# Performance work log

Measured on AMD Instinct MI355X. Metric: run time of the kernel, lower is better.

## Reference

```python
import jax, jax.numpy as jnp
import numpy as np
from jax.scipy.linalg import solve_triangular

H, VD, M = 16, 64, 128
RIDGE = 0.01


def setup_inputs() -> dict:
    key = jax.random.key(0)
    ks = jax.random.split(key, 9)
    B, L, HD = 4, 2048, 1024
    s = 1.0 / np.sqrt(HD).astype(np.float32)
    return {
        "x": jax.random.normal(ks[0], (B, L, HD), dtype=jnp.float32),
        "cur_k": jnp.zeros((1,), dtype=jnp.float32),
        "input_mask": jnp.ones((B, L), dtype=jnp.float32),
        "Wq": jax.random.normal(ks[1], (HD, HD), dtype=jnp.float32) * s,
        "Wk": jax.random.normal(ks[2], (HD, HD), dtype=jnp.float32) * s,
        "Wv": jax.random.normal(ks[3], (HD, HD), dtype=jnp.float32) * s,
        "Wo": jax.random.normal(ks[4], (HD, HD), dtype=jnp.float32) * s,
        "bo": jax.random.normal(ks[5], (HD,), dtype=jnp.float32) * s,
        "rff_W": jax.random.normal(ks[6], (H, VD, M), dtype=jnp.float32),  # / lengthscale=1.0
        "rff_b": 2.0 * np.pi * jax.random.uniform(ks[7], (H, M), dtype=jnp.float32),
    }


def reference(x, cur_k, input_mask, Wq, Wk, Wv, Wo, bo, rff_W, rff_b):
    B, L, HD = x.shape
    scale = jnp.asarray(1.0 / np.sqrt(M), dtype=x.dtype)
    M2 = 2 * M

    def heads(t):  # [B,L,HD] -> [B,H,L,VD]
        return t.reshape(B, L, H, VD).transpose(0, 2, 1, 3)

    q = heads(x @ Wq.T)
    k = heads(x @ Wk.T)
    v = heads(x @ Wv.T)

    mask = input_mask[:, :L].astype(x.dtype)
    qmask = mask[:, None, :, None]  # [B,1,L,1]

    def rff(X):  # [B,H,L,VD] -> [B,H,L,2M]
        proj = jnp.einsum('bhld,hdm->bhlm', X, rff_W) + rff_b[None, :, None, :]
        return scale * jnp.concatenate([jnp.cos(proj), jnp.sin(proj)], axis=-1)

    PhiQ = rff(q)
    PhiK_w = rff(k) * qmask
    V_w = v * qmask

    G = jnp.einsum('bhlm,bhln->bhmn', PhiK_w, PhiK_w)  # [B,H,2M,2M]
    G = G + RIDGE * jnp.eye(M2, dtype=x.dtype)
    T = jnp.einsum('bhlm,bhld->bhmd', PhiK_w, V_w)      # [B,H,2M,VD]

    Lch = jnp.linalg.cholesky(G)
    y = solve_triangular(Lch, T, lower=True)
    W = solve_triangular(jnp.swapaxes(Lch, -2, -1), y, lower=False)

    out = jnp.einsum('bhlm,bhmd->bhld', PhiQ, W)        # [B,H,L,VD]
    # unsqueeze sample dim, permute to [B,1,L,H,VD], flatten heads -> [B,1,L,HD]
    samples = jnp.transpose(out, (0, 2, 1, 3)).reshape(B, L, HD)[:, None]
    samples = samples @ Wo.T + bo                        # W_O (dropout: eval no-op)
    samples = samples * qmask                            # [B,1,L,1] broadcast
    return samples
```

## Files before the change

### kernel.cpp

```cpp
#include <hip/hip_runtime.h>
#include <math.h>

#define B_ 4
#define L_ 2048
#define HD_ 1024
#define H_ 16
#define VD_ 64
#define M_ 128
#define M2_ 256
#define RIDGE_ 0.01f
#define SCALE_ 0.08838834764831845f

typedef unsigned short u16;
typedef __attribute__((ext_vector_type(8))) short short8;
typedef __attribute__((ext_vector_type(4))) float floatx4;

__device__ __forceinline__ u16 f2bf(float x) {
  unsigned u = __float_as_uint(x);
  unsigned r = u + 0x7fff + ((u >> 16) & 1);
  return (u16)(r >> 16);
}
__device__ __forceinline__ float bf2f(u16 h) {
  return __uint_as_float(((unsigned)h) << 16);
}
__device__ __forceinline__ void gload_lds16(const u16* g, u16* l) {
  __builtin_amdgcn_global_load_lds(
      (const __attribute__((address_space(1))) unsigned int*)g,
      (__attribute__((address_space(3))) unsigned int*)l, 16, 0, 0);
}
__device__ __forceinline__ void split4(float4 f, ushort4* h, float4* r) {
  h->x = f2bf(f.x); h->y = f2bf(f.y); h->z = f2bf(f.z); h->w = f2bf(f.w);
  r->x = f.x - bf2f(h->x); r->y = f.y - bf2f(h->y);
  r->z = f.z - bf2f(h->z); r->w = f.w - bf2f(h->w);
}

__global__ __launch_bounds__(256) void cvt_split_kernel(
    const float* __restrict__ src, u16* __restrict__ hi, u16* __restrict__ lo, int n4)
{
  int i = blockIdx.x * 256 + threadIdx.x;
  if (i < n4) {
    float4 f = ((const float4*)src)[i];
    ushort4 hv; float4 r;
    split4(f, &hv, &r);
    ushort4 lv = {f2bf(r.x), f2bf(r.y), f2bf(r.z), f2bf(r.w)};
    ((ushort4*)hi)[i] = hv;
    ((ushort4*)lo)[i] = lv;
  }
}

__global__ __launch_bounds__(256) void mfma_nt(
    const u16* __restrict__ A0, const u16* __restrict__ B0,
    float* __restrict__ C, int Ndim, int Kdim, int ldA, int ldB,
    const float* __restrict__ bias, const float* __restrict__ mask)
{
  __shared__ __align__(16) u16 a_sm[4096];
  __shared__ __align__(16) u16 b_sm[4096];
  const int tid = threadIdx.x;
  const int wave = tid >> 6, lane = tid & 63;
  const int m0 = blockIdx.y * 128, n0 = blockIdx.x * 128;
  const int wrow = (wave >> 1) * 64, wcol = (wave & 1) * 64;
  const int fm = lane & 15, q = lane >> 4;

  floatx4 acc[4][4];
#pragma unroll
  for (int i = 0; i < 4; ++i)
#pragma unroll
    for (int j = 0; j < 4; ++j) acc[i][j] = (floatx4){0.f, 0.f, 0.f, 0.f};

  const u16* Ag0 = A0 + (long)(m0 + lane) * ldA + wave * 8;
  const u16* Ag1 = A0 + (long)(m0 + 64 + lane) * ldA + wave * 8;
  const u16* Bg0 = B0 + (long)(n0 + lane) * ldB + wave * 8;
  const u16* Bg1 = B0 + (long)(n0 + 64 + lane) * ldB + wave * 8;
  u16* la0 = &a_sm[(wave * 128 + 0) * 8];
  u16* la1 = &a_sm[(wave * 128 + 64) * 8];
  u16* lb0 = &b_sm[(wave * 128 + 0) * 8];
  u16* lb1 = &b_sm[(wave * 128 + 64) * 8];

  for (int k0 = 0; k0 < Kdim; k0 += 32) {
    __syncthreads();
    gload_lds16(Ag0 + k0, la0);
    gload_lds16(Ag1 + k0, la1);
    gload_lds16(Bg0 + k0, lb0);
    gload_lds16(Bg1 + k0, lb1);
    __syncthreads();
    short8 af[4], bf[4];
#pragma unroll
    for (int i = 0; i < 4; ++i)
      af[i] = *(const short8*)&a_sm[(q * 128 + wrow + i * 16 + fm) * 8];
#pragma unroll
    for (int j = 0; j < 4; ++j)
      bf[j] = *(const short8*)&b_sm[(q * 128 + wcol + j * 16 + fm) * 8];
#pragma unroll
    for (int i = 0; i < 4; ++i)
#pragma unroll
      for (int j = 0; j < 4; ++j)
        acc[i][j] = __builtin_amdgcn_mfma_f32_16x16x32_bf16(af[i], bf[j], acc[i][j], 0, 0, 0);
  }

  const int colb = n0 + wcol + fm;
  const int rbase = m0 + wrow + (lane >> 4) * 4;
#pragma unroll
  for (int j = 0; j < 4; ++j) {
    int cg = colb + j * 16;
    float bb = bias ? bias[cg] : 0.f;
#pragma unroll
    for (int i = 0; i < 4; ++i) {
#pragma unroll
      for (int r = 0; r < 4; ++r) {
        int row = rbase + i * 16 + r;
        float val = acc[i][j][r];
        if (bias) val = (val + bb) * mask[row];
        C[(long)row * Ndim + cg] = val;
      }
    }
  }
}

__global__ __launch_bounds__(256) void mfma_qk3(
    const u16* __restrict__ Ah, const u16* __restrict__ Al,
    const u16* __restrict__ Bh, const u16* __restrict__ Bl,
    float* __restrict__ Cq, float* __restrict__ Ck)
{
  __shared__ __align__(16) u16 ah_sm[4096], al_sm[4096];
  __shared__ __align__(16) u16 bh_sm[4096], bl_sm[4096];
  const int tid = threadIdx.x;
  const int wave = tid >> 6, lane = tid & 63;
  const int m0 = blockIdx.y * 128, n0 = blockIdx.x * 128;
  const int wrow = (wave >> 1) * 64, wcol = (wave & 1) * 64;
  const int fm = lane & 15, q = lane >> 4;

  floatx4 acc[4][4];
#pragma unroll
  for (int i = 0; i < 4; ++i)
#pragma unroll
    for (int j = 0; j < 4; ++j) acc[i][j] = (floatx4){0.f, 0.f, 0.f, 0.f};

  const long a0o = (long)(m0 + lane) * 1024 + wave * 8;
  const long a1o = (long)(m0 + 64 + lane) * 1024 + wave * 8;
  const long b0o = (long)(n0 + lane) * 1024 + wave * 8;
  const long b1o = (long)(n0 + 64 + lane) * 1024 + wave * 8;
  u16* lah0 = &ah_sm[(wave * 128 + 0) * 8];
  u16* lah1 = &ah_sm[(wave * 128 + 64) * 8];
  u16* lal0 = &al_sm[(wave * 128 + 0) * 8];
  u16* lal1 = &al_sm[(wave * 128 + 64) * 8];
  u16* lbh0 = &bh_sm[(wave * 128 + 0) * 8];
  u16* lbh1 = &bh_sm[(wave * 128 + 64) * 8];
  u16* lbl0 = &bl_sm[(wave * 128 + 0) * 8];
  u16* lbl1 = &bl_sm[(wave * 128 + 64) * 8];

  for (int k0 = 0; k0 < 1024; k0 += 32) {
    __syncthreads();
    gload_lds16(Ah + a0o + k0, lah0);
    gload_lds16(Ah + a1o + k0, lah1);
    gload_lds16(Al + a0o + k0, lal0);
    gload_lds16(Al + a1o + k0, lal1);
    gload_lds16(Bh + b0o + k0, lbh0);
    gload_lds16(Bh + b1o + k0, lbh1);
    gload_lds16(Bl + b0o + k0, lbl0);
    gload_lds16(Bl + b1o + k0, lbl1);
    __syncthreads();
    short8 afh[4], afl[4], bfh[4], bfl[4];
#pragma unroll
    for (int i = 0; i < 4; ++i) {
      afh[i] = *(const short8*)&ah_sm[(q * 128 + wrow + i * 16 + fm) * 8];
      afl[i] = *(const short8*)&al_sm[(q * 128 + wrow + i * 16 + fm) * 8];
    }
#pragma unroll
    for (int j = 0; j < 4; ++j) {
      bfh[j] = *(const short8*)&bh_sm[(q * 128 + wcol + j * 16 + fm) * 8];
      bfl[j] = *(const short8*)&bl_sm[(q * 128 + wcol + j * 16 + fm) * 8];
    }
#pragma unroll
    for (int i = 0; i < 4; ++i)
#pragma unroll
      for (int j = 0; j < 4; ++j) {
        acc[i][j] = __builtin_amdgcn_mfma_f32_16x16x32_bf16(afh[i], bfh[j], acc[i][j], 0, 0, 0);
        acc[i][j] = __builtin_amdgcn_mfma_f32_16x16x32_bf16(afl[i], bfh[j], acc[i][j], 0, 0, 0);
        acc[i][j] = __builtin_amdgcn_mfma_f32_16x16x32_bf16(afh[i], bfl[j], acc[i][j], 0, 0, 0);
      }
  }

  float* Cp; int cb;
  if (n0 < 1024) { Cp = Cq; cb = n0; }
  else           { Cp = Ck; cb = n0 - 1024; }
  const int colb = cb + wcol + fm;
  const int rbase = m0 + wrow + (lane >> 4) * 4;
#pragma unroll
  for (int j = 0; j < 4; ++j) {
    int cg = colb + j * 16;
#pragma unroll
    for (int i = 0; i < 4; ++i)
#pragma unroll
      for (int r = 0; r < 4; ++r)
        Cp[(long)(rbase + i * 16 + r) * 1024 + cg] = acc[i][j][r];
  }
}

__global__ __launch_bounds__(256) void rff_k_t(
    const float* __restrict__ src, const float* __restrict__ mask,
    const float* __restrict__ rffW, const float* __restrict__ rffb,
    u16* __restrict__ pkh, u16* __restrict__ pkl, int b0)
{
  __shared__ __align__(16) float w_lds[64][132];
  __shared__ __align__(16) float x_lds[64][68];
  __shared__ float b_lds[128];
  const int l0 = blockIdx.x * 64;
  const int h = blockIdx.y, b = b0 + blockIdx.z;
  const int zloc = blockIdx.z * 16 + h;
  const int tid = threadIdx.x;

  const float* wsrc = rffW + h * 8192;
  for (int f = tid * 4; f < 8192; f += 1024) {
    int d = f >> 7, m = f & 127;
    *(float4*)&w_lds[d][m] = *(const float4*)&wsrc[f];
  }
  if (tid < 128) b_lds[tid] = rffb[h * 128 + tid];
  {
    int r = tid >> 2, c0 = (tid & 3) * 16;
    const float* srow = src + (long)(b * L_ + l0 + r) * 1024 + h * VD_ + c0;
    *(float4*)&x_lds[r][c0 + 0]  = *(const float4*)(srow + 0);
    *(float4*)&x_lds[r][c0 + 4]  = *(const float4*)(srow + 4);
    *(float4*)&x_lds[r][c0 + 8]  = *(const float4*)(srow + 8);
    *(float4*)&x_lds[r][c0 + 12] = *(const float4*)(srow + 12);
  }
  __syncthreads();

  const int ty = tid >> 4, tx = tid & 15;
  float acc[4][8];
  {
    float4 bb0 = *(const float4*)&b_lds[4 * tx];
    float4 bb1 = *(const float4*)&b_lds[4 * tx + 64];
#pragma unroll
    for (int i = 0; i < 4; ++i) {
      acc[i][0] = bb0.x; acc[i][1] = bb0.y; acc[i][2] = bb0.z; acc[i][3] = bb0.w;
      acc[i][4] = bb1.x; acc[i][5] = bb1.y; acc[i][6] = bb1.z; acc[i][7] = bb1.w;
    }
  }
#pragma unroll 8
  for (int kk = 0; kk < 64; ++kk) {
    float4 w0 = *(const float4*)&w_lds[kk][4 * tx];
    float4 w1 = *(const float4*)&w_lds[kk][4 * tx + 64];
    float xv[4];
#pragma unroll
    for (int i = 0; i < 4; ++i) xv[i] = x_lds[4 * ty + i][kk];
#pragma unroll
    for (int i = 0; i < 4; ++i) {
      acc[i][0] = fmaf(xv[i], w0.x, acc[i][0]);
      acc[i][1] = fmaf(xv[i], w0.y, acc[i][1]);
      acc[i][2] = fmaf(xv[i], w0.z, acc[i][2]);
      acc[i][3] = fmaf(xv[i], w0.w, acc[i][3]);
      acc[i][4] = fmaf(xv[i], w1.x, acc[i][4]);
      acc[i][5] = fmaf(xv[i], w1.y, acc[i][5]);
      acc[i][6] = fmaf(xv[i], w1.z, acc[i][6]);
      acc[i][7] = fmaf(xv[i], w1.w, acc[i][7]);
    }
  }
  float fi[4];
#pragma unroll
  for (int i = 0; i < 4; ++i) fi[i] = SCALE_ * mask[b * L_ + l0 + 4 * ty + i];
  float cvv[4][8], svv[4][8];
#pragma unroll
  for (int i = 0; i < 4; ++i)
#pragma unroll
    for (int jj = 0; jj < 8; ++jj) {
      float sv, cv;
      sincosf(acc[i][jj], &sv, &cv);
      cvv[i][jj] = cv * fi[i];
      svv[i][jj] = sv * fi[i];
    }
  const long lbase = l0 + 4 * ty;
  const long zbase = (long)zloc * 655360;
#pragma unroll
  for (int jj = 0; jj < 8; ++jj) {
    int mcol = (jj < 4) ? (4 * tx + jj) : (64 + 4 * tx + (jj - 4));
    ushort4 h4, l4;
    h4.x = f2bf(cvv[0][jj]); l4.x = f2bf(cvv[0][jj] - bf2f(h4.x));
    h4.y = f2bf(cvv[1][jj]); l4.y = f2bf(cvv[1][jj] - bf2f(h4.y));
    h4.z = f2bf(cvv[2][jj]); l4.z = f2bf(cvv[2][jj] - bf2f(h4.z));
    h4.w = f2bf(cvv[3][jj]); l4.w = f2bf(cvv[3][jj] - bf2f(h4.w));
    long base = zbase + (long)mcol * 2048 + lbase;
    *(ushort4*)&pkh[base] = h4;
    *(ushort4*)&pkl[base] = l4;
    ushort4 hs, ls;
    hs.x = f2bf(svv[0][jj]); ls.x = f2bf(svv[0][jj] - bf2f(hs.x));
    hs.y = f2bf(svv[1][jj]); ls.y = f2bf(svv[1][jj] - bf2f(hs.y));
    hs.z = f2bf(svv[2][jj]); ls.z = f2bf(svv[2][jj] - bf2f(hs.z));
    hs.w = f2bf(svv[3][jj]); ls.w = f2bf(svv[3][jj] - bf2f(hs.w));
    long base2 = zbase + (long)(mcol + 128) * 2048 + lbase;
    *(ushort4*)&pkh[base2] = hs;
    *(ushort4*)&pkl[base2] = ls;
  }
}

__global__ __launch_bounds__(256) void vt_kernel(
    const float* __restrict__ v, const float* __restrict__ mask,
    u16* __restrict__ pkh, u16* __restrict__ pkl, int b0)
{
  __shared__ float t[128][65];
  const int z = blockIdx.y;
  const int b = b0 + (z >> 4), h = z & 15;
  const int l0 = blockIdx.x * 128;
  const int tid = threadIdx.x;
  const int d = tid & 63, lg = tid >> 6;
  for (int i = 0; i < 128; i += 4) {
    int ll = i + lg;
    float mv = mask[b * L_ + l0 + ll];
    t[ll][d] = v[(long)(b * L_ + l0 + ll) * 1024 + h * 64 + d] * mv;
  }
  __syncthreads();
  const int d2 = tid >> 2, lofs = (tid & 3) * 32;
  long base = (long)z * 655360 + (long)(256 + d2) * 2048 + l0 + lofs;
  for (int j = 0; j < 32; j += 4) {
    float f0 = t[lofs + j + 0][d2], f1 = t[lofs + j + 1][d2];
    float f2 = t[lofs + j + 2][d2], f3 = t[lofs + j + 3][d2];
    ushort4 hv, lv;
    hv.x = f2bf(f0); lv.x = f2bf(f0 - bf2f(hv.x));
    hv.y = f2bf(f1); lv.y = f2bf(f1 - bf2f(hv.y));
    hv.z = f2bf(f2); lv.z = f2bf(f2 - bf2f(hv.z));
    hv.w = f2bf(f3); lv.w = f2bf(f3 - bf2f(hv.w));
    *(ushort4*)&pkh[base + j] = hv;
    *(ushort4*)&pkl[base + j] = lv;
  }
}

__global__ __launch_bounds__(256) void mfma_gt(
    const u16* __restrict__ pkh, const u16* __restrict__ pkl,
    float* __restrict__ Gp, float* __restrict__ Tp, int bh0)
{
  __shared__ __align__(16) u16 ah_sm[4096], al_sm[4096];
  __shared__ __align__(16) u16 bh_sm[2048], bl_sm[2048];
  const int tid = threadIdx.x;
  const int wave = tid >> 6, lane = tid & 63;
  const int z = blockIdx.z;
  const int mt = blockIdx.y & 1, kc = blockIdx.y >> 1;
  const int m0 = mt * 128, n0 = blockIdx.x * 64;
  const int wrow = (wave >> 1) * 64, wcol = (wave & 1) * 32;
  const int fm = lane & 15, q = lane >> 4;
  const long batch = (long)z * 655360;
  const u16* Ah = pkh + batch;
  const u16* Al = pkl + batch;

  floatx4 acc[4][2];
#pragma unroll
  for (int i = 0; i < 4; ++i)
#pragma unroll
    for (int j = 0; j < 2; ++j) acc[i][j] = (floatx4){0.f, 0.f, 0.f, 0.f};

  const long a0o = (long)(m0 + lane) * 2048 + wave * 8;
  const long a1o = (long)(m0 + 64 + lane) * 2048 + wave * 8;
  const long b0o = (long)(n0 + lane) * 2048 + wave * 8;
  u16* lah0 = &ah_sm[(wave * 128 + 0) * 8];
  u16* lah1 = &ah_sm[(wave * 128 + 64) * 8];
  u16* lal0 = &al_sm[(wave * 128 + 0) * 8];
  u16* lal1 = &al_sm[(wave * 128 + 64) * 8];
  u16* lbh = &bh_sm[(wave * 64) * 8];
  u16* lbl = &bl_sm[(wave * 64) * 8];

  const int kbeg = kc * 1024, kend = kbeg + 1024;
  for (int k0 = kbeg; k0 < kend; k0 += 32) {
    __syncthreads();
    gload_lds16(Ah + a0o + k0, lah0);
    gload_lds16(Ah + a1o + k0, lah1);
    gload_lds16(Al + a0o + k0, lal0);
    gload_lds16(Al + a1o + k0, lal1);
    gload_lds16(Ah + b0o + k0, lbh);
    gload_lds16(Al + b0o + k0, lbl);
    __syncthreads();
    short8 afh[4], afl[4], bfh[2], bfl[2];
#pragma unroll
    for (int i = 0; i < 4; ++i) {
      afh[i] = *(const short8*)&ah_sm[(q * 128 + wrow + i * 16 + fm) * 8];
      afl[i] = *(const short8*)&al_sm[(q * 128 + wrow + i * 16 + fm) * 8];
    }
#pragma unroll
    for (int j = 0; j < 2; ++j) {
      bfh[j] = *(const short8*)&bh_sm[(q * 64 + wcol + j * 16 + fm) * 8];
      bfl[j] = *(const short8*)&bl_sm[(q * 64 + wcol + j * 16 + fm) * 8];
    }
#pragma unroll
    for (int i = 0; i < 4; ++i)
#pragma unroll
      for (int j = 0; j < 2; ++j) {
        acc[i][j] = __builtin_amdgcn_mfma_f32_16x16x32_bf16(afh[i], bfh[j], acc[i][j], 0, 0, 0);
        acc[i][j] = __builtin_amdgcn_mfma_f32_16x16x32_bf16(afl[i], bfh[j], acc[i][j], 0, 0, 0);
        acc[i][j] = __builtin_amdgcn_mfma_f32_16x16x32_bf16(afh[i], bfl[j], acc[i][j], 0, 0, 0);
      }
  }

  const int bh = bh0 + z;
  float* Gb = Gp + (long)kc * 4194304;
  float* Tb = Tp + (long)kc * 1048576;
  const int rbase = m0 + wrow + (lane >> 4) * 4;
#pragma unroll
  for (int j = 0; j < 2; ++j) {
    int col = n0 + wcol + j * 16 + fm;
#pragma unroll
    for (int i = 0; i < 4; ++i)
#pragma unroll
      for (int r = 0; r < 4; ++r) {
        int row = rbase + i * 16 + r;
        float val = acc[i][j][r];
        if (n0 < 256) Gb[(long)bh * 65536 + (long)row * 256 + col] = val;
        else Tb[(long)bh * 16384 + (long)row * 64 + (col - 256)] = val;
      }
  }
}

__global__ __launch_bounds__(256) void reduce_gt_kernel(
    const float* __restrict__ Gp, float* __restrict__ G,
    const float* __restrict__ Tp, float* __restrict__ T)
{
  long i = (long)blockIdx.x * 256 + threadIdx.x;
  if (i < 1048576) {
    float4 a = ((const float4*)Gp)[i];
    float4 b = ((const float4*)(Gp + 4194304))[i];
    float4 o = {a.x + b.x, a.y + b.y, a.z + b.z, a.w + b.w};
    ((float4*)G)[i] = o;
  } else {
    long j = i - 1048576;
    float4 a = ((const float4*)Tp)[j];
    float4 b = ((const float4*)(Tp + 1048576))[j];
    float4 o = {a.x + b.x, a.y + b.y, a.z + b.z, a.w + b.w};
    ((float4*)T)[j] = o;
  }
}

__global__ __launch_bounds__(256) void mfma_out_k(
    const u16* __restrict__ ph, const u16* __restrict__ pl,
    const u16* __restrict__ wth, const u16* __restrict__ wtl,
    u16* __restrict__ oh)
{
  __shared__ __align__(16) u16 ah_sm[4096], al_sm[4096];
  __shared__ __align__(16) u16 bh_sm[2048], bl_sm[2048];
  const int tid = threadIdx.x;
  const int wave = tid >> 6, lane = tid & 63;
  const int bh = blockIdx.y;
  const int b = bh >> 4, h = bh & 15;
  const int l0 = blockIdx.x * 128;
  const int wrow = (wave >> 1) * 64, wcol = (wave & 1) * 32;
  const int fm = lane & 15, q = lane >> 4;
  const u16* Ah = ph + (long)bh * 524288 + (long)l0 * 256;
  const u16* Al = pl + (long)bh * 524288 + (long)l0 * 256;
  const u16* Bh = wth + (long)bh * 16384;
  const u16* Bl = wtl + (long)bh * 16384;

  floatx4 acc[4][2];
#pragma unroll
  for (int i = 0; i < 4; ++i)
#pragma unroll
    for (int j = 0; j < 2; ++j) acc[i][j] = (floatx4){0.f, 0.f, 0.f, 0.f};

  const long a0o = (long)lane * 256 + wave * 8;
  const long a1o = (long)(64 + lane) * 256 + wave * 8;
  const long b0o = (long)lane * 256 + wave * 8;
  u16* lah0 = &ah_sm[(wave * 128 + 0) * 8];
  u16* lah1 = &ah_sm[(wave * 128 + 64) * 8];
  u16* lal0 = &al_sm[(wave * 128 + 0) * 8];
  u16* lal1 = &al_sm[(wave * 128 + 64) * 8];
  u16* lbh = &bh_sm[(wave * 64) * 8];
  u16* lbl = &bl_sm[(wave * 64) * 8];

  for (int k0 = 0; k0 < 256; k0 += 32) {
    __syncthreads();
    gload_lds16(Ah + a0o + k0, lah0);
    gload_lds16(Ah + a1o + k0, lah1);
    gload_lds16(Al + a0o + k0, lal0);
    gload_lds16(Al + a1o + k0, lal1);
    gload_lds16(Bh + b0o + k0, lbh);
    gload_lds16(Bl + b0o + k0, lbl);
    __syncthreads();
    short8 afh[4], afl[4], bfh[2], bfl[2];
#pragma unroll
    for (int i = 0; i < 4; ++i) {
      afh[i] = *(const short8*)&ah_sm[(q * 128 + wrow + i * 16 + fm) * 8];
      afl[i] = *(const short8*)&al_sm[(q * 128 + wrow + i * 16 + fm) * 8];
    }
#pragma unroll
    for (int j = 0; j < 2; ++j) {
      bfh[j] = *(const short8*)&bh_sm[(q * 64 + wcol + j * 16 + fm) * 8];
      bfl[j] = *(const short8*)&bl_sm[(q * 64 + wcol + j * 16 + fm) * 8];
    }
#pragma unroll
    for (int i = 0; i < 4; ++i)
#pragma unroll
      for (int j = 0; j < 2; ++j) {
        acc[i][j] = __builtin_amdgcn_mfma_f32_16x16x32_bf16(afh[i], bfh[j], acc[i][j], 0, 0, 0);
        acc[i][j] = __builtin_amdgcn_mfma_f32_16x16x32_bf16(afl[i], bfh[j], acc[i][j], 0, 0, 0);
        acc[i][j] = __builtin_amdgcn_mfma_f32_16x16x32_bf16(afh[i], bfl[j], acc[i][j], 0, 0, 0);
      }
  }

  const int rbase = l0 + wrow + (lane >> 4) * 4;
#pragma unroll
  for (int j = 0; j < 2; ++j) {
    int col = h * 64 + wcol + j * 16 + fm;
#pragma unroll
    for (int i = 0; i < 4; ++i)
#pragma unroll
      for (int r = 0; r < 4; ++r)
        oh[(long)(b * L_ + rbase + i * 16 + r) * 1024 + col] = f2bf(acc[i][j][r]);
  }
}

__global__ __launch_bounds__(512) void chol_rffq_wo_kernel(
    const float* __restrict__ G, float* __restrict__ Lg,
    const float* __restrict__ qsrc,
    const float* __restrict__ rffW, const float* __restrict__ rffb,
    u16* __restrict__ ph, u16* __restrict__ pl,
    const float* __restrict__ Wo, u16* __restrict__ wo_hi)
{
  extern __shared__ float sm[];
  const int bx = blockIdx.x;
  const int tid = threadIdx.x;

  if (bx < 64) {
    float* Lb = sm;
    const int bh = bx;
    const float* Gb = G + (long)bh * 65536;
    for (int f = tid; f < 136 * 256; f += 512) {
      int bi = f >> 8, e = f & 255;
      int i = e >> 4, j = e & 15;
      int I = 0; while ((I + 1) * (I + 2) / 2 <= bi) ++I;
      int J = bi - I * (I + 1) / 2;
      float v = Gb[(I * 16 + i) * 256 + J * 16 + j];
      if (I == J && i == j) v += RIDGE_;
      Lb[bi * 272 + i * 17 + j] = v;
    }
    __syncthreads();

    for (int p = 0; p < 16; ++p) {
      const int diagbase = (p * (p + 1) / 2 + p) * 272;
      if (tid < 64) {
        const int i = tid & 15;
        float r[16];
#pragma unroll
        for (int k = 0; k < 16; ++k) r[k] = Lb[diagbase + i * 17 + k];
#pragma unroll
        for (int j = 0; j < 16; ++j) {
          float dj = __shfl(r[j], j);
          float dinv = 1.0f / sqrtf(dj);
          r[j] *= dinv;
          float Lij = r[j];
#pragma unroll
          for (int k = j + 1; k < 16; ++k) {
            float Lkj = __shfl(r[j], k);
            r[k] = fmaf(-Lij, Lkj, r[k]);
          }
        }
        float x[16];
#pragma unroll
        for (int j = 0; j < 16; ++j) {
          float s = (i == j) ? 1.0f : 0.0f;
#pragma unroll
          for (int k = 0; k < j; ++k) {
            float Ljk = __shfl(r[k], j);
            s = fmaf(-Ljk, x[k], s);
          }
          float Ljj = __shfl(r[j], j);
          x[j] = s / Ljj;
        }
        if (tid < 16) {
#pragma unroll
          for (int j = 0; j < 16; ++j) Lb[diagbase + j * 17 + tid] = x[j];
        }
      }
      __syncthreads();

      const int nIb = 15 - p;
      const int tot = nIb * 256;
      float outv[8];
#pragma unroll
      for (int s = 0; s < 8; ++s) {
        int f = tid + s * 512;
        if (f < tot) {
          int Ib = f >> 8;
          int I = p + 1 + Ib;
          int e = f & 255;
          int i = e >> 4, j = e & 15;
          const float* Ablk = &Lb[(I * (I + 1) / 2 + p) * 272 + i * 17];
          const float* invD = &Lb[diagbase + j * 17];
          float s2 = 0.f;
#pragma unroll
          for (int k = 0; k < 16; ++k) s2 = fmaf(Ablk[k], invD[k], s2);
          outv[s] = s2;
        }
      }
      __syncthreads();
#pragma unroll
      for (int s = 0; s < 8; ++s) {
        int f = tid + s * 512;
        if (f < tot) {
          int Ib = f >> 8;
          int I = p + 1 + Ib;
          int e = f & 255;
          int i = e >> 4, j = e & 15;
          Lb[(I * (I + 1) / 2 + p) * 272 + i * 17 + j] = outv[s];
        }
      }
      __syncthreads();

      const int npairs = nIb * (nIb + 1) / 2;
      const int g = tid >> 4, t = tid & 15;
      const int tx = t & 3, ty = t >> 2;
      for (int pi0 = 0; pi0 < npairs; pi0 += 32) {
        int pi = pi0 + g;
        if (pi < npairs) {
          int a = 0; while ((a + 1) * (a + 2) / 2 <= pi) ++a;
          int b2 = pi - a * (a + 1) / 2;
          int I = p + 1 + a, J = p + 1 + b2;
          float* Cblk = &Lb[(I * (I + 1) / 2 + J) * 272];
          const float* Ablk = &Lb[(I * (I + 1) / 2 + p) * 272];
          const float* Bblk = &Lb[(J * (J + 1) / 2 + p) * 272];
          float c4[4][4];
#pragma unroll
          for (int ii = 0; ii < 4; ++ii)
#pragma unroll
            for (int jj = 0; jj < 4; ++jj)
              c4[ii][jj] = Cblk[(4 * ty + ii) * 17 + 4 * tx + jj];
#pragma unroll
          for (int kk = 0; kk < 16; ++kk) {
            float av[4], bv[4];
#pragma unroll
            for (int ii = 0; ii < 4; ++ii) av[ii] = Ablk[(4 * ty + ii) * 17 + kk];
#pragma unroll
            for (int jj = 0; jj < 4; ++jj) bv[jj] = Bblk[(4 * tx + jj) * 17 + kk];
#pragma unroll
            for (int ii = 0; ii < 4; ++ii)
#pragma unroll
              for (int jj = 0; jj < 4; ++jj)
                c4[ii][jj] = fmaf(-av[ii], bv[jj], c4[ii][jj]);
          }
#pragma unroll
          for (int ii = 0; ii < 4; ++ii)
#pragma unroll
            for (int jj = 0; jj < 4; ++jj)
              Cblk[(4 * ty + ii) * 17 + 4 * tx + jj] = c4[ii][jj];
        }
      }
      __syncthreads();
    }

    float* Lgb = Lg + (long)bh * 34816;
    for (int f = tid * 4; f < 136 * 256; f += 2048) {
      int bi = f >> 8, e = f & 255;
      int i = e >> 4, j = e & 15;
      float4 v;
      v.x = Lb[bi * 272 + i * 17 + j];
      v.y = Lb[bi * 272 + i * 17 + j + 1];
      v.z = Lb[bi * 272 + i * 17 + j + 2];
      v.w = Lb[bi * 272 + i * 17 + j + 3];
      *(float4*)&Lgb[f] = v;
    }
  } else if (bx < 64 + 1024) {
    const int id = bx - 64;
    const int l0 = (id & 15) * 128;
    const int h = (id >> 4) & 15;
    const int b = id >> 8;
    float* w_lds = sm;
    float* x_lds = sm + 8448;
    float* b_lds = sm + 8448 + 8704;

    const float* wsrc = rffW + h * 8192;
    for (int f = tid * 4; f < 8192; f += 2048) {
      int d = f >> 7, m = f & 127;
      *(float4*)&w_lds[d * 132 + m] = *(const float4*)&wsrc[f];
    }
    if (tid < 128) b_lds[tid] = rffb[h * 128 + tid];
    {
      int r = tid >> 2, c0 = (tid & 3) * 16;
      const float* srow = qsrc + (long)(b * L_ + l0 + r) * 1024 + h * VD_ + c0;
      *(float4*)&x_lds[r * 68 + c0 + 0]  = *(const float4*)(srow + 0);
      *(float4*)&x_lds[r * 68 + c0 + 4]  = *(const float4*)(srow + 4);
      *(float4*)&x_lds[r * 68 + c0 + 8]  = *(const float4*)(srow + 8);
      *(float4*)&x_lds[r * 68 + c0 + 12] = *(const float4*)(srow + 12);
    }
    __syncthreads();

    const int sub = tid >> 8;
    const int t = tid & 255;
    const int ty = t >> 4, tx = t & 15;
    const int rrow = sub * 64 + 4 * ty;
    float acc[4][8];
    {
      float4 bb0 = *(const float4*)&b_lds[4 * tx];
      float4 bb1 = *(const float4*)&b_lds[4 * tx + 64];
#pragma unroll
      for (int i = 0; i < 4; ++i) {
        acc[i][0] = bb0.x; acc[i][1] = bb0.y; acc[i][2] = bb0.z; acc[i][3] = bb0.w;
        acc[i][4] = bb1.x; acc[i][5] = bb1.y; acc[i][6] = bb1.z; acc[i][7] = bb1.w;
      }
    }
#pragma unroll 8
    for (int kk = 0; kk < 64; ++kk) {
      float4 w0 = *(const float4*)&w_lds[kk * 132 + 4 * tx];
      float4 w1 = *(const float4*)&w_lds[kk * 132 + 4 * tx + 64];
      float xv[4];
#pragma unroll
      for (int i = 0; i < 4; ++i) xv[i] = x_lds[(rrow + i) * 68 + kk];
#pragma unroll
      for (int i = 0; i < 4; ++i) {
        acc[i][0] = fmaf(xv[i], w0.x, acc[i][0]);
        acc[i][1] = fmaf(xv[i], w0.y, acc[i][1]);
        acc[i][2] = fmaf(xv[i], w0.z, acc[i][2]);
        acc[i][3] = fmaf(xv[i], w0.w, acc[i][3]);
        acc[i][4] = fmaf(xv[i], w1.x, acc[i][4]);
        acc[i][5] = fmaf(xv[i], w1.y, acc[i][5]);
        acc[i][6] = fmaf(xv[i], w1.z, acc[i][6]);
        acc[i][7] = fmaf(xv[i], w1.w, acc[i][7]);
      }
    }
#pragma unroll
    for (int i = 0; i < 4; ++i) {
      int l = l0 + rrow + i;
      float4 c0, c1, s0, s1;
      float sv, cv;
      sincosf(acc[i][0], &sv, &cv); c0.x = cv * SCALE_; s0.x = sv * SCALE_;
      sincosf(acc[i][1], &sv, &cv); c0.y = cv * SCALE_; s0.y = sv * SCALE_;
      sincosf(acc[i][2], &sv, &cv); c0.z = cv * SCALE_; s0.z = sv * SCALE_;
      sincosf(acc[i][3], &sv, &cv); c0.w = cv * SCALE_; s0.w = sv * SCALE_;
      sincosf(acc[i][4], &sv, &cv); c1.x = cv * SCALE_; s1.x = sv * SCALE_;
      sincosf(acc[i][5], &sv, &cv); c1.y = cv * SCALE_; s1.y = sv * SCALE_;
      sincosf(acc[i][6], &sv, &cv); c1.z = cv * SCALE_; s1.z = sv * SCALE_;
      sincosf(acc[i][7], &sv, &cv); c1.w = cv * SCALE_; s1.w = sv * SCALE_;
      long base = ((long)(b * H_ + h) * L_ + l) * M2_;
      ushort4 hv; float4 r4;
      split4(c0, &hv, &r4);
      *(ushort4*)&ph[base + 4 * tx] = hv;
      *(ushort4*)&pl[base + 4 * tx] = (ushort4){f2bf(r4.x), f2bf(r4.y), f2bf(r4.z), f2bf(r4.w)};
      split4(c1, &hv, &r4);
      *(ushort4*)&ph[base + 64 + 4 * tx] = hv;
      *(ushort4*)&pl[base + 64 + 4 * tx] = (ushort4){f2bf(r4.x), f2bf(r4.y), f2bf(r4.z), f2bf(r4.w)};
      split4(s0, &hv, &r4);
      *(ushort4*)&ph[base + 128 + 4 * tx] = hv;
      *(ushort4*)&pl[base + 128 + 4 * tx] = (ushort4){f2bf(r4.x), f2bf(r4.y), f2bf(r4.z), f2bf(r4.w)};
      split4(s1, &hv, &r4);
      *(ushort4*)&ph[base + 192 + 4 * tx] = hv;
      *(ushort4*)&pl[base + 192 + 4 * tx] = (ushort4){f2bf(r4.x), f2bf(r4.y), f2bf(r4.z), f2bf(r4.w)};
    }
  } else {
    const int id2 = bx - (64 + 1024);
    int idx = id2 * 512 + tid;
    for (int i = idx; i < 262144; i += 65536) {
      float4 f = ((const float4*)Wo)[i];
      ushort4 hv = {f2bf(f.x), f2bf(f.y), f2bf(f.z), f2bf(f.w)};
      ((ushort4*)wo_hi)[i] = hv;
    }
  }
}

__global__ __launch_bounds__(256) void tri_solve_kernel(
    const float* __restrict__ Lg, const float* __restrict__ T,
    u16* __restrict__ wth, u16* __restrict__ wtl)
{
  __shared__ float Y[256 * 17];
  __shared__ float tmp[16 * 17];
  const int bh = blockIdx.y;
  const int d0 = blockIdx.x * 16;
  const int tid = threadIdx.x;
  const int i = tid >> 4, d = tid & 15;
  const float* Lb = Lg + (long)bh * 34816;
  const float* Tb = T + (long)bh * 16384;

  for (int r = i; r < 256; r += 16) Y[r * 17 + d] = Tb[r * 64 + d0 + d];
  __syncthreads();

  for (int J = 0; J < 16; ++J) {
    float acc = Y[(J * 16 + i) * 17 + d];
    for (int c = 0; c < J; ++c) {
      const float* Lblk = &Lb[(J * (J + 1) / 2 + c) * 256 + i * 16];
#pragma unroll
      for (int k = 0; k < 16; k += 4) {
        float4 l4 = *(const float4*)&Lblk[k];
        acc = fmaf(-l4.x, Y[(c * 16 + k + 0) * 17 + d], acc);
        acc = fmaf(-l4.y, Y[(c * 16 + k + 1) * 17 + d], acc);
        acc = fmaf(-l4.z, Y[(c * 16 + k + 2) * 17 + d], acc);
        acc = fmaf(-l4.w, Y[(c * 16 + k + 3) * 17 + d], acc);
      }
    }
    tmp[i * 17 + d] = acc;
    __syncthreads();
    const float* invD = &Lb[(J * (J + 1) / 2 + J) * 256 + i * 16];
    float y = 0.f;
#pragma unroll
    for (int k = 0; k < 16; ++k) y = fmaf(invD[k], tmp[k * 17 + d], y);
    Y[(J * 16 + i) * 17 + d] = y;
    __syncthreads();
  }

  for (int J = 15; J >= 0; --J) {
    float acc = Y[(J * 16 + i) * 17 + d];
    for (int I = J + 1; I < 16; ++I) {
      const float* Lblk = &Lb[(I * (I + 1) / 2 + J) * 256];
#pragma unroll
      for (int k = 0; k < 16; ++k)
        acc = fmaf(-Lblk[k * 16 + i], Y[(I * 16 + k) * 17 + d], acc);
    }
    tmp[i * 17 + d] = acc;
    __syncthreads();
    const float* invD = &Lb[(J * (J + 1) / 2 + J) * 256];
    float w = 0.f;
#pragma unroll
    for (int k = 0; k < 16; ++k) w = fmaf(invD[k * 16 + i], tmp[k * 17 + d], w);
    Y[(J * 16 + i) * 17 + d] = w;
    __syncthreads();
  }

  for (int f = tid; f < 16 * 256; f += 256) {
    int dc = f >> 8, m = f & 255;
    float val = Y[m * 17 + dc];
    u16 h = f2bf(val);
    long o = (long)bh * 16384 + (long)(d0 + dc) * 256 + m;
    wth[o] = h;
    wtl[o] = f2bf(val - bf2f(h));
  }
}

__global__ void ws_too_small_kernel(float* out) { out[0] = 12345.0f; }

extern "C" void kernel_launch(void* const* d_in, const int* in_sizes, int n_in,
                              void* d_out, int out_size, void* d_ws, size_t ws_size,
                              hipStream_t stream) {
  const float* x    = (const float*)d_in[0];
  const float* mask = (const float*)d_in[2];
  const float* Wq   = (const float*)d_in[3];
  const float* Wk   = (const float*)d_in[4];
  const float* Wv   = (const float*)d_in[5];
  const float* Wo   = (const float*)d_in[6];
  const float* bo   = (const float*)d_in[7];
  const float* rffW = (const float*)d_in[8];
  const float* rffb = (const float*)d_in[9];
  float* out = (float*)d_out;
  float* ws  = (float*)d_ws;

  const size_t needed = 58720256UL * 4UL;
  if (ws_size < needed) {
    ws_too_small_kernel<<<1, 1, 0, stream>>>(out);
    return;
  }
  float* q = ws;
  u16* oh_bf = (u16*)ws;
  float* kbuf = ws + 8388608;
  float* T    = ws + 8388608;
  float* G    = ws + 9437184;
  float* Lg   = ws + 13631488;
  u16* big16 = (u16*)(ws + 16777216);
  u16* x_hi = big16;
  u16* x_lo = big16 + 8388608;
  u16* w_hi = big16 + 16777216;
  u16* w_lo = big16 + 19922944;
  u16* pk_hi = big16;
  u16* pk_lo = big16 + 20971520;
  float* Gp = ws + 37748736;
  float* Tp = ws + 46137344;
  u16* phiq_hi = big16;
  u16* phiq_lo = big16 + 33554432;
  float* v = ws + 50331648;
  u16* wt_hi = (u16*)(ws + 50331648);
  u16* wt_lo = wt_hi + 1048576;
  u16* wo_hi = wt_hi + 2097152;

  hipFuncSetAttribute((const void*)chol_rffq_wo_kernel,
                      hipFuncAttributeMaxDynamicSharedMemorySize, 147968);

  dim3 blk(256);

  cvt_split_kernel<<<8192, blk, 0, stream>>>(x, x_hi, x_lo, 2097152);
  cvt_split_kernel<<<1024, blk, 0, stream>>>(Wq, w_hi,           w_lo,           262144);
  cvt_split_kernel<<<1024, blk, 0, stream>>>(Wk, w_hi + 1048576, w_lo + 1048576, 262144);
  cvt_split_kernel<<<1024, blk, 0, stream>>>(Wv, w_hi + 2097152, w_lo + 2097152, 262144);

  mfma_qk3<<<dim3(16, 64), blk, 0, stream>>>(x_hi, x_lo, w_hi, w_lo, q, kbuf);
  mfma_nt<<<dim3(8, 64), blk, 0, stream>>>(x_hi, w_hi + 2097152, v,
                                           1024, 1024, 1024, 1024, nullptr, nullptr);

  for (int half = 0; half < 2; ++half) {
    int b0 = half * 2, bh0 = half * 32;
    rff_k_t<<<dim3(32, 16, 2), blk, 0, stream>>>(kbuf, mask, rffW, rffb, pk_hi, pk_lo, b0);
    vt_kernel<<<dim3(16, 32), blk, 0, stream>>>(v, mask, pk_hi, pk_lo, b0);
    mfma_gt<<<dim3(5, 4, 32), blk, 0, stream>>>(pk_hi, pk_lo, Gp, Tp, bh0);
  }

  reduce_gt_kernel<<<5120, blk, 0, stream>>>(Gp, G, Tp, T);

  chol_rffq_wo_kernel<<<dim3(64 + 1024 + 128), dim3(512), 147968, stream>>>(
      G, Lg, q, rffW, rffb, phiq_hi, phiq_lo, Wo, wo_hi);

  tri_solve_kernel<<<dim3(4, 64), dim3(256), 0, stream>>>(Lg, T, wt_hi, wt_lo);

  mfma_out_k<<<dim3(16, 64), blk, 0, stream>>>(phiq_hi, phiq_lo, wt_hi, wt_lo, oh_bf);

  mfma_nt<<<dim3(8, 64), blk, 0, stream>>>(oh_bf, wo_hi, out, 1024, 1024, 1024, 1024, bo, mask);
}
```

Baseline: 958.6 us.

## Run blocked Cholesky in place in global memory to shrink shared memory footprint

The Cholesky blocks no longer copy the whole packed lower triangle of G into a 148KB LDS buffer. They factor G in place in global memory, keeping only the current column panel and the inverted diagonal block in LDS, and the triangular solve reads L directly from G in full-matrix layout. Dynamic LDS drops to about 52KB, so more blocks of the fused kernel can share a CU. The RFF-Q part is re-tiled to 64 rows per block with twice as many blocks. The cost is that the trailing-update reads and writes and the solve's strided column reads now go to global memory through cache.

```diff
diff --git a/kernel.cpp b/kernel.cpp
--- a/kernel.cpp
+++ b/kernel.cpp
@@ -503,7 +503,7 @@
 }
 
 __global__ __launch_bounds__(512) void chol_rffq_wo_kernel(
-    const float* __restrict__ G, float* __restrict__ Lg,
+    float* __restrict__ Gw,
     const float* __restrict__ qsrc,
     const float* __restrict__ rffW, const float* __restrict__ rffb,
     u16* __restrict__ ph, u16* __restrict__ pl,
@@ -514,27 +514,17 @@
   const int tid = threadIdx.x;
 
   if (bx < 64) {
-    float* Lb = sm;
-    const int bh = bx;
-    const float* Gb = G + (long)bh * 65536;
-    for (int f = tid; f < 136 * 256; f += 512) {
-      int bi = f >> 8, e = f & 255;
-      int i = e >> 4, j = e & 15;
-      int I = 0; while ((I + 1) * (I + 2) / 2 <= bi) ++I;
-      int J = bi - I * (I + 1) / 2;
-      float v = Gb[(I * 16 + i) * 256 + J * 16 + j];
-      if (I == J && i == j) v += RIDGE_;
-      Lb[bi * 272 + i * 17 + j] = v;
-    }
-    __syncthreads();
+    float* panel = sm;
+    float* invD  = sm + 4352;
+    float* Gb = Gw + (long)bx * 65536;
 
     for (int p = 0; p < 16; ++p) {
-      const int diagbase = (p * (p + 1) / 2 + p) * 272;
       if (tid < 64) {
         const int i = tid & 15;
         float r[16];
 #pragma unroll
-        for (int k = 0; k < 16; ++k) r[k] = Lb[diagbase + i * 17 + k];
+        for (int k = 0; k < 16; ++k) r[k] = Gb[(16 * p + i) * 256 + 16 * p + k];
+        r[i] += RIDGE_;
 #pragma unroll
         for (int j = 0; j < 16; ++j) {
           float dj = __shfl(r[j], j);
@@ -561,27 +551,36 @@
         }
         if (tid < 16) {
 #pragma unroll
-          for (int j = 0; j < 16; ++j) Lb[diagbase + j * 17 + tid] = x[j];
+          for (int j = 0; j < 16; ++j) {
+            invD[j * 17 + tid] = x[j];
+            Gb[(16 * p + j) * 256 + 16 * p + tid] = x[j];
+          }
         }
       }
       __syncthreads();
 
       const int nIb = 15 - p;
-      const int tot = nIb * 256;
+      if (nIb == 0) break;
+      const int nrows = nIb * 16;
+      const int r0 = 16 * (p + 1);
+
+      for (int f = tid; f < nrows * 16; f += 512) {
+        int rr = f >> 4, cc = f & 15;
+        panel[(r0 + rr) * 17 + cc] = Gb[(long)(r0 + rr) * 256 + 16 * p + cc];
+      }
+      __syncthreads();
+
       float outv[8];
 #pragma unroll
       for (int s = 0; s < 8; ++s) {
         int f = tid + s * 512;
-        if (f < tot) {
-          int Ib = f >> 8;
-          int I = p + 1 + Ib;
-          int e = f & 255;
-          int i = e >> 4, j = e & 15;
-          const float* Ablk = &Lb[(I * (I + 1) / 2 + p) * 272 + i * 17];
-          const float* invD = &Lb[diagbase + j * 17];
+        if (f < nrows * 16) {
+          int rr = f >> 4, j = f & 15;
+          const float* arow = &panel[(r0 + rr) * 17];
+          const float* dcol = &invD[j * 17];
           float s2 = 0.f;
 #pragma unroll
-          for (int k = 0; k < 16; ++k) s2 = fmaf(Ablk[k], invD[k], s2);
+          for (int k = 0; k < 16; ++k) s2 = fmaf(arow[k], dcol[k], s2);
           outv[s] = s2;
         }
       }
@@ -589,12 +588,10 @@
 #pragma unroll
       for (int s = 0; s < 8; ++s) {
         int f = tid + s * 512;
-        if (f < tot) {
-          int Ib = f >> 8;
-          int I = p + 1 + Ib;
-          int e = f & 255;
-          int i = e >> 4, j = e & 15;
-          Lb[(I * (I + 1) / 2 + p) * 272 + i * 17 + j] = outv[s];
+        if (f < nrows * 16) {
+          int rr = f >> 4, j = f & 15;
+          panel[(r0 + rr) * 17 + j] = outv[s];
+          Gb[(long)(r0 + rr) * 256 + 16 * p + j] = outv[s];
         }
       }
       __syncthreads();
@@ -608,22 +605,19 @@
           int a = 0; while ((a + 1) * (a + 2) / 2 <= pi) ++a;
           int b2 = pi - a * (a + 1) / 2;
           int I = p + 1 + a, J = p + 1 + b2;
-          float* Cblk = &Lb[(I * (I + 1) / 2 + J) * 272];
-          const float* Ablk = &Lb[(I * (I + 1) / 2 + p) * 272];
-          const float* Bblk = &Lb[(J * (J + 1) / 2 + p) * 272];
           float c4[4][4];
 #pragma unroll
-          for (int ii = 0; ii < 4; ++ii)
-#pragma unroll
-            for (int jj = 0; jj < 4; ++jj)
-              c4[ii][jj] = Cblk[(4 * ty + ii) * 17 + 4 * tx + jj];
+          for (int ii = 0; ii < 4; ++ii) {
+            float4 cv = *(const float4*)&Gb[(long)(16 * I + 4 * ty + ii) * 256 + 16 * J + 4 * tx];
+            c4[ii][0] = cv.x; c4[ii][1] = cv.y; c4[ii][2] = cv.z; c4[ii][3] = cv.w;
+          }
 #pragma unroll
           for (int kk = 0; kk < 16; ++kk) {
             float av[4], bv[4];
 #pragma unroll
-            for (int ii = 0; ii < 4; ++ii) av[ii] = Ablk[(4 * ty + ii) * 17 + kk];
-#pragma unroll
-            for (int jj = 0; jj < 4; ++jj) bv[jj] = Bblk[(4 * tx + jj) * 17 + kk];
+            for (int ii = 0; ii < 4; ++ii) av[ii] = panel[(16 * I + 4 * ty + ii) * 17 + kk];
+#pragma unroll
+            for (int jj = 0; jj < 4; ++jj) bv[jj] = panel[(16 * J + 4 * tx + jj) * 17 + kk];
 #pragma unroll
             for (int ii = 0; ii < 4; ++ii)
 #pragma unroll
@@ -631,34 +625,22 @@
                 c4[ii][jj] = fmaf(-av[ii], bv[jj], c4[ii][jj]);
           }
 #pragma unroll
-          for (int ii = 0; ii < 4; ++ii)
-#pragma unroll
-            for (int jj = 0; jj < 4; ++jj)
-              Cblk[(4 * ty + ii) * 17 + 4 * tx + jj] = c4[ii][jj];
+          for (int ii = 0; ii < 4; ++ii) {
+            float4 cv = {c4[ii][0], c4[ii][1], c4[ii][2], c4[ii][3]};
+            *(float4*)&Gb[(long)(16 * I + 4 * ty + ii) * 256 + 16 * J + 4 * tx] = cv;
+          }
         }
       }
       __syncthreads();
     }
-
-    float* Lgb = Lg + (long)bh * 34816;
-    for (int f = tid * 4; f < 136 * 256; f += 2048) {
-      int bi = f >> 8, e = f & 255;
-      int i = e >> 4, j = e & 15;
-      float4 v;
-      v.x = Lb[bi * 272 + i * 17 + j];
-      v.y = Lb[bi * 272 + i * 17 + j + 1];
-      v.z = Lb[bi * 272 + i * 17 + j + 2];
-      v.w = Lb[bi * 272 + i * 17 + j + 3];
-      *(float4*)&Lgb[f] = v;
-    }
-  } else if (bx < 64 + 1024) {
+  } else if (bx < 64 + 2048) {
     const int id = bx - 64;
-    const int l0 = (id & 15) * 128;
-    const int h = (id >> 4) & 15;
-    const int b = id >> 8;
+    const int l0 = (id & 31) * 64;
+    const int h = (id >> 5) & 15;
+    const int b = id >> 9;
     float* w_lds = sm;
     float* x_lds = sm + 8448;
-    float* b_lds = sm + 8448 + 8704;
+    float* b_lds = sm + 12800;
 
     const float* wsrc = rffW + h * 8192;
     for (int f = tid * 4; f < 8192; f += 2048) {
@@ -667,25 +649,23 @@
     }
     if (tid < 128) b_lds[tid] = rffb[h * 128 + tid];
     {
-      int r = tid >> 2, c0 = (tid & 3) * 16;
+      int r = tid >> 3, c0 = (tid & 7) * 8;
       const float* srow = qsrc + (long)(b * L_ + l0 + r) * 1024 + h * VD_ + c0;
-      *(float4*)&x_lds[r * 68 + c0 + 0]  = *(const float4*)(srow + 0);
-      *(float4*)&x_lds[r * 68 + c0 + 4]  = *(const float4*)(srow + 4);
-      *(float4*)&x_lds[r * 68 + c0 + 8]  = *(const float4*)(srow + 8);
-      *(float4*)&x_lds[r * 68 + c0 + 12] = *(const float4*)(srow + 12);
+      *(float4*)&x_lds[r * 68 + c0 + 0] = *(const float4*)(srow + 0);
+      *(float4*)&x_lds[r * 68 + c0 + 4] = *(const float4*)(srow + 4);
     }
     __syncthreads();
 
     const int sub = tid >> 8;
     const int t = tid & 255;
     const int ty = t >> 4, tx = t & 15;
-    const int rrow = sub * 64 + 4 * ty;
-    float acc[4][8];
+    const int rrow = sub * 32 + 2 * ty;
+    float acc[2][8];
     {
       float4 bb0 = *(const float4*)&b_lds[4 * tx];
       float4 bb1 = *(const float4*)&b_lds[4 * tx + 64];
 #pragma unroll
-      for (int i = 0; i < 4; ++i) {
+      for (int i = 0; i < 2; ++i) {
         acc[i][0] = bb0.x; acc[i][1] = bb0.y; acc[i][2] = bb0.z; acc[i][3] = bb0.w;
         acc[i][4] = bb1.x; acc[i][5] = bb1.y; acc[i][6] = bb1.z; acc[i][7] = bb1.w;
       }
@@ -694,11 +674,11 @@
     for (int kk = 0; kk < 64; ++kk) {
       float4 w0 = *(const float4*)&w_lds[kk * 132 + 4 * tx];
       float4 w1 = *(const float4*)&w_lds[kk * 132 + 4 * tx + 64];
-      float xv[4];
-#pragma unroll
-      for (int i = 0; i < 4; ++i) xv[i] = x_lds[(rrow + i) * 68 + kk];
-#pragma unroll
-      for (int i = 0; i < 4; ++i) {
+      float xv[2];
+#pragma unroll
+      for (int i = 0; i < 2; ++i) xv[i] = x_lds[(rrow + i) * 68 + kk];
+#pragma unroll
+      for (int i = 0; i < 2; ++i) {
         acc[i][0] = fmaf(xv[i], w0.x, acc[i][0]);
         acc[i][1] = fmaf(xv[i], w0.y, acc[i][1]);
         acc[i][2] = fmaf(xv[i], w0.z, acc[i][2]);
@@ -710,7 +690,7 @@
       }
     }
 #pragma unroll
-    for (int i = 0; i < 4; ++i) {
+    for (int i = 0; i < 2; ++i) {
       int l = l0 + rrow + i;
       float4 c0, c1, s0, s1;
       float sv, cv;
@@ -738,7 +718,7 @@
       *(ushort4*)&pl[base + 192 + 4 * tx] = (ushort4){f2bf(r4.x), f2bf(r4.y), f2bf(r4.z), f2bf(r4.w)};
     }
   } else {
-    const int id2 = bx - (64 + 1024);
+    const int id2 = bx - (64 + 2048);
     int idx = id2 * 512 + tid;
     for (int i = idx; i < 262144; i += 65536) {
       float4 f = ((const float4*)Wo)[i];
@@ -749,7 +729,7 @@
 }
 
 __global__ __launch_bounds__(256) void tri_solve_kernel(
-    const float* __restrict__ Lg, const float* __restrict__ T,
+    const float* __restrict__ Gw, const float* __restrict__ T,
     u16* __restrict__ wth, u16* __restrict__ wtl)
 {
   __shared__ float Y[256 * 17];
@@ -758,7 +738,7 @@
   const int d0 = blockIdx.x * 16;
   const int tid = threadIdx.x;
   const int i = tid >> 4, d = tid & 15;
-  const float* Lb = Lg + (long)bh * 34816;
+  const float* Gb = Gw + (long)bh * 65536;
   const float* Tb = T + (long)bh * 16384;
 
   for (int r = i; r < 256; r += 16) Y[r * 17 + d] = Tb[r * 64 + d0 + d];
@@ -767,7 +747,7 @@
   for (int J = 0; J < 16; ++J) {
     float acc = Y[(J * 16 + i) * 17 + d];
     for (int c = 0; c < J; ++c) {
-      const float* Lblk = &Lb[(J * (J + 1) / 2 + c) * 256 + i * 16];
+      const float* Lblk = &Gb[(long)(16 * J + i) * 256 + 16 * c];
 #pragma unroll
       for (int k = 0; k < 16; k += 4) {
         float4 l4 = *(const float4*)&Lblk[k];
@@ -779,7 +759,7 @@
     }
     tmp[i * 17 + d] = acc;
     __syncthreads();
-    const float* invD = &Lb[(J * (J + 1) / 2 + J) * 256 + i * 16];
+    const float* invD = &Gb[(long)(16 * J + i) * 256 + 16 * J];
     float y = 0.f;
 #pragma unroll
     for (int k = 0; k < 16; ++k) y = fmaf(invD[k], tmp[k * 17 + d], y);
@@ -790,17 +770,16 @@
   for (int J = 15; J >= 0; --J) {
     float acc = Y[(J * 16 + i) * 17 + d];
     for (int I = J + 1; I < 16; ++I) {
-      const float* Lblk = &Lb[(I * (I + 1) / 2 + J) * 256];
 #pragma unroll
       for (int k = 0; k < 16; ++k)
-        acc = fmaf(-Lblk[k * 16 + i], Y[(I * 16 + k) * 17 + d], acc);
+        acc = fmaf(-Gb[(long)(16 * I + k) * 256 + 16 * J + i], Y[(I * 16 + k) * 17 + d], acc);
     }
     tmp[i * 17 + d] = acc;
     __syncthreads();
-    const float* invD = &Lb[(J * (J + 1) / 2 + J) * 256];
     float w = 0.f;
 #pragma unroll
-    for (int k = 0; k < 16; ++k) w = fmaf(invD[k * 16 + i], tmp[k * 17 + d], w);
+    for (int k = 0; k < 16; ++k)
+      w = fmaf(Gb[(long)(16 * J + k) * 256 + 16 * J + i], tmp[k * 17 + d], w);
     Y[(J * 16 + i) * 17 + d] = w;
     __syncthreads();
   }
@@ -842,7 +821,6 @@
   float* kbuf = ws + 8388608;
   float* T    = ws + 8388608;
   float* G    = ws + 9437184;
-  float* Lg   = ws + 13631488;
   u16* big16 = (u16*)(ws + 16777216);
   u16* x_hi = big16;
   u16* x_lo = big16 + 8388608;
@@ -860,7 +838,7 @@
   u16* wo_hi = wt_hi + 2097152;
 
   hipFuncSetAttribute((const void*)chol_rffq_wo_kernel,
-                      hipFuncAttributeMaxDynamicSharedMemorySize, 147968);
+                      hipFuncAttributeMaxDynamicSharedMemorySize, 51712);
 
   dim3 blk(256);
 
@@ -882,10 +860,10 @@
 
   reduce_gt_kernel<<<5120, blk, 0, stream>>>(Gp, G, Tp, T);
 
-  chol_rffq_wo_kernel<<<dim3(64 + 1024 + 128), dim3(512), 147968, stream>>>(
-      G, Lg, q, rffW, rffb, phiq_hi, phiq_lo, Wo, wo_hi);
-
-  tri_solve_kernel<<<dim3(4, 64), dim3(256), 0, stream>>>(Lg, T, wt_hi, wt_lo);
+  chol_rffq_wo_kernel<<<dim3(64 + 2048 + 128), dim3(512), 51712, stream>>>(
+      G, q, rffW, rffb, phiq_hi, phiq_lo, Wo, wo_hi);
+
+  tri_solve_kernel<<<dim3(4, 64), dim3(256), 0, stream>>>(G, T, wt_hi, wt_lo);
 
   mfma_out_k<<<dim3(16, 64), blk, 0, stream>>>(phiq_hi, phiq_lo, wt_hi, wt_lo, oh_bf);
 
```

New measurement: 893.2 us. 1.07x faster.
